# Optimization experiments

Measured on AMD Instinct MI355X. Metric: run time of the kernel, lower is better.

## Reference

```python
import jax, jax.numpy as jnp
from jax import lax
import numpy as np

B, C2, H2, W2 = 16, 512, 28, 28
C3, H3, W3 = 1024, 14, 14
N_CORESET, EMB = 16384, C2 + C3
IMG = 224
NUM_NEIGHBORS = 9
SIGMA = 4.0
KS = 2 * int(4.0 * SIGMA + 0.5) + 1  # kornia default kernel size = 33


def setup_inputs() -> dict:
    key = jax.random.key(0)
    k1, k2, k3 = jax.random.split(key, 3)
    return {
        "feat_layer2": jax.random.normal(k1, (B, C2, H2, W2), jnp.float32),
        "feat_layer3": jax.random.normal(k2, (B, C3, H3, W3), jnp.float32),
        "embedding_coreset": jax.random.normal(k3, (N_CORESET, EMB), jnp.float32),
    }


def avg_pool3(x):
    # torch.nn.AvgPool2d(3, 1, 1), count_include_pad=True -> always divide by 9
    s = lax.reduce_window(x, 0.0, lax.add, (1, 1, 3, 3), (1, 1, 1, 1),
                          [(0, 0), (0, 0), (1, 1), (1, 1)])
    return s / 9.0


def cdist(a, b):
    # euclidean cdist: [Q,E] x [N,E] -> [Q,N]
    a2 = jnp.sum(a * a, axis=-1, keepdims=True)          # [Q,1]
    b2 = jnp.sum(b * b, axis=-1)[None, :]                # [1,N]
    d2 = a2 + b2 - 2.0 * (a @ b.T)
    return jnp.sqrt(jnp.maximum(d2, 1e-12))


def gaussian_blur(x):
    # kornia GaussianBlur2d(kernel=33, sigma=4, border='reflect'), separable
    half = (KS - 1) // 2
    t = jnp.arange(KS, dtype=x.dtype) - half
    k = jnp.exp(-(t * t) / (2.0 * SIGMA * SIGMA))
    k = k / jnp.sum(k)
    xp = jnp.pad(x, ((0, 0), (0, 0), (half, half), (half, half)), mode="reflect")
    dn = ("NCHW", "OIHW", "NCHW")
    y = lax.conv_general_dilated(xp, k.reshape(1, 1, KS, 1), (1, 1), "VALID", dimension_numbers=dn)
    y = lax.conv_general_dilated(y, k.reshape(1, 1, 1, KS), (1, 1), "VALID", dimension_numbers=dn)
    return y


def reference(feat_layer2, feat_layer3, embedding_coreset):
    # 1. feature pooling (AvgPool2d(3,1,1)) on each backbone layer
    p2 = avg_pool3(feat_layer2)                           # [B,512,28,28]
    p3 = avg_pool3(feat_layer3)                           # [B,1024,14,14]
    p3u = jnp.repeat(jnp.repeat(p3, 2, axis=2), 2, axis=3)  # [B,1024,28,28]
    embedding = jnp.concatenate([p2, p3u], axis=1)        # [B,1536,28,28]
    b, e, w, h = embedding.shape
    x = embedding.transpose(0, 2, 3, 1).reshape(-1, e)    # [B*28*28, 1536]

    # 3. nearest neighbor (n_neighbors=1) against the coreset
    dists = cdist(x, embedding_coreset)                   # [Q, N]
    patch_scores = jnp.min(dists, axis=1).reshape(b, -1)  # [B, P]
    locations = jnp.argmin(dists, axis=1).reshape(b, -1)  # [B, P]

    # 4. image-level anomaly score with num_neighbors=9 reweighting
    bidx = jnp.arange(b)
    max_patches = jnp.argmax(patch_scores, axis=1)        # [B]
    mpf = x.reshape(b, w * h, e)[bidx, max_patches]       # [B, E]
    score = patch_scores[bidx, max_patches]               # [B]
    nn_index = locations[bidx, max_patches]               # [B]
    nn_sample = embedding_coreset[nn_index]               # [B, E]
    d2 = cdist(nn_sample, embedding_coreset)              # [B, N]
    _, support = lax.top_k(-d2, NUM_NEIGHBORS)            # smallest 9, ascending
    sup_feats = embedding_coreset[support]                # [B, 9, E]
    diff = mpf[:, None, :] - sup_feats
    d_sup = jnp.sqrt(jnp.maximum(jnp.sum(diff * diff, axis=-1), 1e-12))  # [B, 9]
    weights = (1.0 - jax.nn.softmax(d_sup, axis=1))[:, 0]
    anomaly_score = weights * score                       # [B]

    # 5. anomaly map: bilinear upsample + gaussian blur
    sm = patch_scores.reshape(b, 1, w, h)
    sm = jax.image.resize(sm, (b, 1, IMG, IMG), method="bilinear")
    anomaly_map = gaussian_blur(sm)                       # [B,1,224,224]
    return anomaly_map, anomaly_score
```

## Files before the change

### kernel.cpp

```cpp
#include <hip/hip_runtime.h>
#include <math.h>

typedef unsigned char u8;
typedef unsigned short u16;
typedef unsigned int u32;
typedef unsigned long long u64;
typedef __attribute__((ext_vector_type(8))) int int8v;
typedef __attribute__((ext_vector_type(4))) int int4v;
typedef __attribute__((ext_vector_type(4))) float f32x4;

#define B_IMG 16
#define EMB 1536
#define NPATCH 784
#define Q_TOT (B_IMG * NPATCH)
#define NCORE 16384
#define BK 128
#define IMG 224
#define KS 33
#define HALF 16
#define REFINE_W 12.0f

#define BM 256
#define BN 256
#define MBLK (Q_TOT / BM)
#define NBLK2 (NCORE / BN)
#define NHALF 256


__device__ __forceinline__ u32 fkey(float f) {
    u32 u = __float_as_uint(f);
    return (u & 0x80000000u) ? ~u : (u | 0x80000000u);
}
__device__ __forceinline__ float fkey_inv(u32 k) {
    u32 u = (k & 0x80000000u) ? (k ^ 0x80000000u) : ~k;
    return __uint_as_float(u);
}

__device__ __forceinline__ u32 f2e4m3(float f) {
    u32 x = __float_as_uint(f);
    u32 sign = (x >> 24) & 0x80u;
    x &= 0x7fffffffu;
    if (x >= 0x43E00000u) return sign | 0x7Eu;
    u32 e = x >> 23;
    if (e >= 121) {
        u32 m = x & 0x7fffffu;
        u32 keep = m >> 20;
        u32 rest = m & 0xFFFFFu;
        u32 rnd = (rest > 0x80000u) || (rest == 0x80000u && (keep & 1u));
        u32 mant = keep + rnd;
        u32 e4 = e - 120;
        if (mant == 8) { mant = 0; e4 += 1; }
        return sign | (e4 << 3) | mant;
    }
    float a = __uint_as_float(x);
    u32 q = (u32)(a * 512.0f + 0.5f);
    if (q > 7) return sign | 0x08u;
    return sign | q;
}

__device__ __forceinline__ void async_copy16(const void* gsrc, void* ldst) {
    auto g = reinterpret_cast<const __attribute__((address_space(1))) u32*>(
        reinterpret_cast<uintptr_t>(gsrc));
    auto l = reinterpret_cast<__attribute__((address_space(3))) u32*>(
        reinterpret_cast<uintptr_t>(ldst));
    __builtin_amdgcn_global_load_lds(g, l, 16, 0, 0);
}

__global__ void k_split_cs(const float* __restrict__ cs, u8* __restrict__ cs8,
                           float* __restrict__ b2) {
    __shared__ float sm[4];
    const int n = blockIdx.x;
    const int t = threadIdx.x;
    const size_t base = (size_t)n * EMB;
    float s = 0.f;
#pragma unroll
    for (int i = 0; i < 6; ++i) {
        const int e = t + i * 256;
        float v = cs[base + e];
        cs8[base + e] = (u8)f2e4m3(v);
        s += v * v;
    }
#pragma unroll
    for (int off = 32; off > 0; off >>= 1) s += __shfl_down(s, off, 64);
    if ((t & 63) == 0) sm[t >> 6] = s;
    __syncthreads();
    if (t == 0) b2[n] = sm[0] + sm[1] + sm[2] + sm[3];
}

__global__ void k_build_x(const float* __restrict__ f2, const float* __restrict__ f3,
                          u8* __restrict__ x8, float* __restrict__ xf) {
    __shared__ float tile[32][33];
    const int tx = threadIdx.x, ty = threadIdx.y;
    const int hw0 = blockIdx.x * 32;
    const int e0 = blockIdx.y * 32;
    const int b = blockIdx.z;
    const int hw = hw0 + tx;
    const bool ok = hw < NPATCH;
    const int h = hw / 28, w = hw - h * 28;
#pragma unroll
    for (int j = 0; j < 4; ++j) {
        const int el = ty + 8 * j;
        const int e = e0 + el;
        float v = 0.f;
        if (ok) {
            if (e < 512) {
                const float* p = f2 + (size_t)(b * 512 + e) * 784;
#pragma unroll
                for (int dy = -1; dy <= 1; ++dy) {
                    int yy = h + dy;
                    if (yy < 0 || yy >= 28) continue;
#pragma unroll
                    for (int dx = -1; dx <= 1; ++dx) {
                        int xx = w + dx;
                        if (xx < 0 || xx >= 28) continue;
                        v += p[yy * 28 + xx];
                    }
                }
            } else {
                const int c = e - 512;
                const int y3 = h >> 1, x3 = w >> 1;
                const float* p = f3 + (size_t)(b * 1024 + c) * 196;
#pragma unroll
                for (int dy = -1; dy <= 1; ++dy) {
                    int yy = y3 + dy;
                    if (yy < 0 || yy >= 14) continue;
#pragma unroll
                    for (int dx = -1; dx <= 1; ++dx) {
                        int xx = x3 + dx;
                        if (xx < 0 || xx >= 14) continue;
                        v += p[yy * 14 + xx];
                    }
                }
            }
            v *= (1.0f / 9.0f);
        }
        tile[el][tx] = v;
    }
    __syncthreads();
#pragma unroll
    for (int j = 0; j < 4; ++j) {
        const int hwl = ty + 8 * j;
        const int hw2 = hw0 + hwl;
        if (hw2 < NPATCH) {
            const int q = b * NPATCH + hw2;
            const float v = tile[tx][hwl];
            x8[(size_t)q * EMB + e0 + tx] = (u8)f2e4m3(v);
            xf[(size_t)q * EMB + e0 + tx] = v;
        }
    }
}

__global__ __launch_bounds__(512, 2) void k_gemm(
    const u8* __restrict__ x8, const u8* __restrict__ cs8,
    const float* __restrict__ b2, u64* __restrict__ cand) {
    __shared__ __align__(16) u8 sA0[BM * BK];
    __shared__ __align__(16) u8 sA1[BM * BK];
    __shared__ __align__(16) u8 sB0[BN * BK];
    __shared__ __align__(16) u8 sB1[BN * BK];

    const int tid = threadIdx.x;
    const int lane = tid & 63;
    const int wid = tid >> 6;
    const int wy = wid >> 2;
    const int wx = wid & 3;
    const int qd = lane >> 4;
    const int lr = lane & 15;
    const int sw = lr & 7;

    const u32 bid = blockIdx.x;
    const u32 xcd = bid & 7;
    const u32 sl = bid >> 3;
    const int bx = (int)(xcd * 8 + (sl & 7));
    const int by = (int)(sl >> 3);
    const int m0 = by * BM;
    const int n0 = bx * BN;

    size_t srcA[4], srcB[4];
    int dst[4];
#pragma unroll
    for (int j = 0; j < 4; ++j) {
        const int s = tid + j * 512;
        const int r = s >> 3, p = s & 7;
        const int col = (p ^ (r & 7)) << 4;
        srcA[j] = (size_t)(m0 + r) * EMB + col;
        srcB[j] = (size_t)(n0 + r) * EMB + col;
        dst[j] = s << 4;
    }

    f32x4 acc[8][4];
#pragma unroll
    for (int i = 0; i < 8; ++i)
#pragma unroll
        for (int j = 0; j < 4; ++j) acc[i][j] = (f32x4){0.f, 0.f, 0.f, 0.f};

    const int aoff0 = (wy * 128 + lr) * BK + (((qd * 2) ^ sw) << 4);
    const int boff0 = (wx * 64 + lr) * BK + (((qd * 2) ^ sw) << 4);

#define STAGE(SA, SB, KSI) do {                                                \
        const size_t kk_ = (size_t)(KSI) * BK;                                 \
        _Pragma("unroll")                                                      \
        for (int j_ = 0; j_ < 4; ++j_) {                                       \
            async_copy16(x8 + srcA[j_] + kk_, (SA) + dst[j_]);                 \
            async_copy16(cs8 + srcB[j_] + kk_, (SB) + dst[j_]);                \
        }                                                                      \
    } while (0)

#define COMPUTE(SA, SB) do {                                                   \
        int8v a_[8];                                                           \
        _Pragma("unroll")                                                      \
        for (int mi_ = 0; mi_ < 8; ++mi_) {                                    \
            const int o_ = aoff0 + mi_ * (16 * BK);                            \
            *(int4v*)&a_[mi_] = *(const int4v*)((SA) + o_);                    \
            *(((int4v*)&a_[mi_]) + 1) = *(const int4v*)((SA) + (o_ ^ 16));     \
        }                                                                      \
        _Pragma("unroll")                                                      \
        for (int nj_ = 0; nj_ < 4; ++nj_) {                                    \
            const int ob_ = boff0 + nj_ * (16 * BK);                           \
            int8v b_;                                                          \
            *(int4v*)&b_ = *(const int4v*)((SB) + ob_);                        \
            *(((int4v*)&b_) + 1) = *(const int4v*)((SB) + (ob_ ^ 16));         \
            _Pragma("unroll")                                                  \
            for (int mi_ = 0; mi_ < 8; ++mi_)                                  \
                acc[mi_][nj_] = __builtin_amdgcn_mfma_scale_f32_16x16x128_f8f6f4( \
                    a_[mi_], b_, acc[mi_][nj_], 0, 0, 0, 0x7F7F7F7F, 0, 0x7F7F7F7F); \
        }                                                                      \
    } while (0)

    STAGE(sA0, sB0, 0);
    __syncthreads();
    for (int ks = 0; ks < 12; ks += 2) {
        STAGE(sA1, sB1, ks + 1);
        COMPUTE(sA0, sB0);
        __syncthreads();
        if (ks + 2 < 12) STAGE(sA0, sB0, ks + 2);
        COMPUTE(sA1, sB1);
        __syncthreads();
    }
#undef STAGE
#undef COMPUTE

    float bb[4];
#pragma unroll
    for (int nj = 0; nj < 4; ++nj) bb[nj] = b2[n0 + wx * 64 + nj * 16 + lr];

#pragma unroll
    for (int mi = 0; mi < 8; ++mi) {
#pragma unroll
        for (int r = 0; r < 4; ++r) {
            u64 best = ~0ull;
#pragma unroll
            for (int nj = 0; nj < 4; ++nj) {
                const int n_g = n0 + wx * 64 + nj * 16 + lr;
                float v = bb[nj] - 2.0f * acc[mi][nj][r];
                u64 key = ((u64)fkey(v) << 32) | (u32)n_g;
                best = best < key ? best : key;
            }
#pragma unroll
            for (int s = 1; s < 16; s <<= 1) {
                u64 o = __shfl_xor(best, s, 64);
                best = best < o ? best : o;
            }
            if (lr == 0) {
                const int m_l = wy * 128 + mi * 16 + qd * 4 + r;
                cand[(size_t)(m0 + m_l) * NHALF + (bx * 4 + wx)] = best;
            }
        }
    }
}

__global__ void k_refine(const u64* __restrict__ cand, const float* __restrict__ xf,
                         const float* __restrict__ cs,
                         float* __restrict__ scores, int* __restrict__ locs) {
    __shared__ u64 keys[NHALF];
    __shared__ float sx[EMB];
    __shared__ float fred[256];
    __shared__ u64 ured[256];
    __shared__ int clist[16];
    __shared__ int ccount;
    __shared__ float s_a2, s_lim;
    const int row = blockIdx.x;
    const int t = threadIdx.x;
    keys[t] = cand[(size_t)row * NHALF + t];
    float p = 0.f;
    for (int e = t; e < EMB; e += 256) {
        float v = xf[(size_t)row * EMB + e];
        sx[e] = v;
        p += v * v;
    }
    fred[t] = p;
    if (t == 0) ccount = 0;
    __syncthreads();
    for (int s = 128; s > 0; s >>= 1) {
        if (t < s) fred[t] += fred[t + s];
        __syncthreads();
    }
    if (t == 0) s_a2 = fred[0];
    ured[t] = keys[t];
    __syncthreads();
    for (int s = 128; s > 0; s >>= 1) {
        if (t < s) { u64 o = ured[t + s]; if (o < ured[t]) ured[t] = o; }
        __syncthreads();
    }
    if (t == 0) s_lim = s_a2 + fkey_inv((u32)(ured[0] >> 32)) + REFINE_W;
    __syncthreads();
    {
        float d2a = s_a2 + fkey_inv((u32)(keys[t] >> 32));
        if (d2a <= s_lim) {
            int pos = atomicAdd(&ccount, 1);
            if (pos < 16) clist[pos] = (int)(keys[t] & 0xffffffffu);
        }
    }
    __syncthreads();
    const int nc = min(ccount, 16);
    u64 best = ~0ull;
    for (int i = 0; i < nc; ++i) {
        const int n = clist[i];
        const float* c = cs + (size_t)n * EMB;
        float q = 0.f;
        for (int e = t; e < EMB; e += 256) {
            float d = sx[e] - c[e];
            q += d * d;
        }
        fred[t] = q;
        __syncthreads();
        for (int s = 128; s > 0; s >>= 1) {
            if (t < s) fred[t] += fred[t + s];
            __syncthreads();
        }
        if (t == 0) {
            u64 key = ((u64)fkey(fred[0]) << 32) | (u32)n;
            best = best < key ? best : key;
        }
        __syncthreads();
    }
    if (t == 0) {
        float d2 = fkey_inv((u32)(best >> 32));
        scores[row] = sqrtf(fmaxf(d2, 1e-12f));
        locs[row] = (int)(best & 0xffffffffu);
    }
}

__global__ void k_argmax(const float* __restrict__ scores, const int* __restrict__ locs,
                         float* __restrict__ imgscore, int* __restrict__ nnidx,
                         int* __restrict__ qstar) {
    __shared__ u64 red[256];
    const int b = blockIdx.x, t = threadIdx.x;
    u64 best = 0;
    for (int p = t; p < NPATCH; p += 256) {
        u32 u = __float_as_uint(scores[b * NPATCH + p]);
        u64 key = ((u64)u << 32) | (u32)(0xFFFFFFFFu - (u32)p);
        best = best > key ? best : key;
    }
    red[t] = best;
    __syncthreads();
    for (int s = 128; s > 0; s >>= 1) {
        if (t < s) { u64 o = red[t + s]; if (o > red[t]) red[t] = o; }
        __syncthreads();
    }
    if (t == 0) {
        u64 k = red[0];
        int p = (int)(0xFFFFFFFFu - (u32)(k & 0xFFFFFFFFu));
        imgscore[b] = __uint_as_float((u32)(k >> 32));
        nnidx[b] = locs[b * NPATCH + p];
        qstar[b] = b * NPATCH + p;
    }
}

__global__ void k_d2nn(const float* __restrict__ cs, const int* __restrict__ nnidx,
                       float* __restrict__ dpart) {
    __shared__ float snn[16 * 384];
    const int t = threadIdx.x;
    const int nb = blockIdx.x & 63, ksl = blockIdx.x >> 6;
    const int n = nb * 256 + t;
    const int k0 = ksl * 384;
#pragma unroll
    for (int j = 0; j < 6; ++j) {
        int fid = t + j * 256;
        int row = fid / 96;
        int c4 = fid - row * 96;
        ((float4*)snn)[row * 96 + c4] =
            ((const float4*)(cs + (size_t)nnidx[row] * EMB + k0))[c4];
    }
    __syncthreads();
    float acc[16];
#pragma unroll
    for (int b = 0; b < 16; ++b) acc[b] = 0.f;
    const float4* csrow = (const float4*)(cs + (size_t)n * EMB + k0);
    for (int k4 = 0; k4 < 96; ++k4) {
        float4 c4 = csrow[k4];
#pragma unroll
        for (int b = 0; b < 16; ++b) {
            float4 nb4 = ((const float4*)snn)[b * 96 + k4];
            acc[b] += c4.x * nb4.x + c4.y * nb4.y + c4.z * nb4.z + c4.w * nb4.w;
        }
    }
#pragma unroll
    for (int b = 0; b < 16; ++b)
        dpart[((size_t)ksl * 16 + b) * NCORE + n] = acc[b];
}

__global__ void k_topk(const float* __restrict__ dpart, const float* __restrict__ b2,
                       const int* __restrict__ nnidx,
                       const float* __restrict__ cs, const float* __restrict__ xf,
                       const int* __restrict__ qstar, const float* __restrict__ imgscore,
                       float* __restrict__ out_scores) {
    __shared__ float sd2[NCORE];
    __shared__ int sel_idx[9];
    __shared__ float dsup[9];
    __shared__ u64 red[256];
    __shared__ float fred[256];
    const int b = blockIdx.x, t = threadIdx.x;
    const float bnn = b2[nnidx[b]];
    for (int n = t; n < NCORE; n += 256) {
        float dot = dpart[(0 * 16 + b) * NCORE + n] + dpart[(1 * 16 + b) * NCORE + n] +
                    dpart[(2 * 16 + b) * NCORE + n] + dpart[(3 * 16 + b) * NCORE + n];
        sd2[n] = bnn + b2[n] - 2.f * dot;
    }
    __syncthreads();

    for (int j = 0; j < 9; ++j) {
        u64 best = ~0ull;
        for (int n = t; n < NCORE; n += 256) {
            u64 key = ((u64)fkey(sd2[n]) << 32) | (u32)n;
            best = best < key ? best : key;
        }
        red[t] = best;
        __syncthreads();
        for (int s = 128; s > 0; s >>= 1) {
            if (t < s) { u64 o = red[t + s]; if (o < red[t]) red[t] = o; }
            __syncthreads();
        }
        if (t == 0) {
            int sel = (int)(red[0] & 0xffffffffu);
            sel_idx[j] = sel;
            sd2[sel] = __uint_as_float(0x7F800000u);
        }
        __syncthreads();
    }

    const int q = qstar[b];
    for (int j = 0; j < 9; ++j) {
        const int s = sel_idx[j];
        float p = 0.f;
        for (int e = t; e < EMB; e += 256) {
            float d = xf[(size_t)q * EMB + e] - cs[(size_t)s * EMB + e];
            p += d * d;
        }
        fred[t] = p;
        __syncthreads();
        for (int ss = 128; ss > 0; ss >>= 1) {
            if (t < ss) fred[t] += fred[t + ss];
            __syncthreads();
        }
        if (t == 0) dsup[j] = sqrtf(fmaxf(fred[0], 1e-12f));
        __syncthreads();
    }

    if (t == 0) {
        float m = dsup[0];
        for (int j = 1; j < 9; ++j) m = fmaxf(m, dsup[j]);
        float se = 0.f, e0 = 0.f;
        for (int j = 0; j < 9; ++j) {
            float e = expf(dsup[j] - m);
            se += e;
            if (j == 0) e0 = e;
        }
        out_scores[b] = (1.0f - e0 / se) * imgscore[b];
    }
}

__global__ void k_bilx(const float* __restrict__ scores, float* __restrict__ Sx) {
    int i = blockIdx.x * 256 + threadIdx.x;
    if (i >= B_IMG * 28 * IMG) return;
    int x = i % IMG;
    int br = i / IMG;
    int r = br % 28, b = br / 28;
    float cx = (x + 0.5f) * 0.125f - 0.5f;
    int x0 = (int)floorf(cx);
    float fx = cx - (float)x0;
    int x1 = min(max(x0 + 1, 0), 27);
    x0 = min(max(x0, 0), 27);
    const float* s = scores + b * NPATCH + r * 28;
    Sx[i] = (1.f - fx) * s[x0] + fx * s[x1];
}

__global__ void k_blur_vf(const float* __restrict__ Sx, float* __restrict__ out1) {
    __shared__ float wv[28];
    const int y = blockIdx.x, b = blockIdx.y, t = threadIdx.x;
    if (t < 28) wv[t] = 0.f;
    __syncthreads();
    if (t == 0) {
        float wsum = 0.f;
        for (int j = 0; j < KS; ++j) {
            float d = (float)(j - HALF);
            wsum += expf(-(d * d) / 32.0f);
        }
        for (int j = 0; j < KS; ++j) {
            int yy = y - HALF + j;
            yy = yy < 0 ? -yy : (yy > 223 ? 446 - yy : yy);
            float cy = (yy + 0.5f) * 0.125f - 0.5f;
            int y0 = (int)floorf(cy);
            float fy = cy - (float)y0;
            int y1 = min(max(y0 + 1, 0), 27);
            y0 = min(max(y0, 0), 27);
            float d = (float)(j - HALF);
            float wkj = expf(-(d * d) / 32.0f) / wsum;
            wv[y0] += (1.f - fy) * wkj;
            wv[y1] += fy * wkj;
        }
    }
    __syncthreads();
    if (t < IMG) {
        float acc = 0.f;
#pragma unroll
        for (int r = 0; r < 28; ++r) acc += wv[r] * Sx[(b * 28 + r) * IMG + t];
        out1[((size_t)b * IMG + y) * IMG + t] = acc;
    }
}

__global__ void k_blur_h(const float* __restrict__ out1, float* __restrict__ out) {
    __shared__ float row[IMG];
    __shared__ float wk[KS];
    const int y = blockIdx.x, b = blockIdx.y, t = threadIdx.x;
    if (t < IMG) row[t] = out1[((size_t)b * IMG + y) * IMG + t];
    if (t < KS) {
        float d = (float)(t - HALF);
        wk[t] = expf(-(d * d) / 32.0f);
    }
    __syncthreads();
    if (t < IMG) {
        float wsum = 0.f, acc = 0.f;
#pragma unroll
        for (int j = 0; j < KS; ++j) wsum += wk[j];
#pragma unroll
        for (int j = 0; j < KS; ++j) {
            int xx = t - HALF + j;
            xx = xx < 0 ? -xx : (xx > 223 ? 446 - xx : xx);
            acc += wk[j] * row[xx];
        }
        out[((size_t)b * IMG + y) * IMG + t] = acc / wsum;
    }
}

extern "C" void kernel_launch(void* const* d_in, const int* in_sizes, int n_in,
                              void* d_out, int out_size, void* d_ws, size_t ws_size,
                              hipStream_t stream) {
    const float* f2 = (const float*)d_in[0];
    const float* f3 = (const float*)d_in[1];
    const float* cs = (const float*)d_in[2];
    float* out = (float*)d_out;

    char* w = (char*)d_ws;
    auto alloc = [&](size_t bytes) {
        char* p = w;
        w += (bytes + 255) & ~(size_t)255;
        return p;
    };
    u8* x8 = (u8*)alloc((size_t)Q_TOT * EMB);
    float* xf = (float*)alloc((size_t)Q_TOT * EMB * 4);
    u8* cs8 = (u8*)alloc((size_t)NCORE * EMB);
    float* b2 = (float*)alloc(NCORE * 4);
    u64* cand = (u64*)alloc((size_t)Q_TOT * NHALF * 8);
    float* scores = (float*)alloc(Q_TOT * 4);
    int* locs = (int*)alloc(Q_TOT * 4);
    float* imgscore = (float*)alloc(B_IMG * 4);
    int* nnidx = (int*)alloc(B_IMG * 4);
    int* qstar = (int*)alloc(B_IMG * 4);
    float* dpart = (float*)alloc((size_t)4 * B_IMG * NCORE * 4);
    float* Sx = (float*)alloc((size_t)B_IMG * 28 * IMG * 4);
    float* map1 = (float*)alloc((size_t)B_IMG * IMG * IMG * 4);

    k_split_cs<<<NCORE, 256, 0, stream>>>(cs, cs8, b2);
    k_build_x<<<dim3(25, 48, 16), dim3(32, 8), 0, stream>>>(f2, f3, x8, xf);
    k_gemm<<<dim3(MBLK * NBLK2), 512, 0, stream>>>(x8, cs8, b2, cand);
    k_refine<<<Q_TOT, 256, 0, stream>>>(cand, xf, cs, scores, locs);
    k_argmax<<<16, 256, 0, stream>>>(scores, locs, imgscore, nnidx, qstar);
    k_d2nn<<<256, 256, 0, stream>>>(cs, nnidx, dpart);
    k_topk<<<16, 256, 0, stream>>>(dpart, b2, nnidx, cs, xf, qstar, imgscore,
                                   out + B_IMG * IMG * IMG);
    k_bilx<<<(B_IMG * 28 * IMG + 255) / 256, 256, 0, stream>>>(scores, Sx);
    k_blur_vf<<<dim3(IMG, B_IMG), 256, 0, stream>>>(Sx, map1);
    k_blur_h<<<dim3(IMG, B_IMG), 256, 0, stream>>>(map1, out);
}
```

Measured before the change: 1.043 ms.

## Interleave LDS loads and MFMA phases with barriers and priority bumps in GEMM loop

Restructures the double-buffered FP8 MFMA main loop so that each k-step issues its async copies, loads A fragments, then alternates B-fragment LDS loads and 8-MFMA groups separated by workgroup barriers and sched_barriers. It raises wave priority around MFMA bursts with s_setprio and waits on vmcnt explicitly before the final barrier. The aim is to keep waves in lockstep so LDS reads from some waves overlap MFMA work from others, ping-pong style. The cost is many extra s_barrier instructions per k-step, which could stall waves if occupancy is low.

```diff
diff --git a/kernel.cpp b/kernel.cpp
--- a/kernel.cpp
+++ b/kernel.cpp
@@ -196,48 +196,86 @@
     const int aoff0 = (wy * 128 + lr) * BK + (((qd * 2) ^ sw) << 4);
     const int boff0 = (wx * 64 + lr) * BK + (((qd * 2) ^ sw) << 4);
 
-#define STAGE(SA, SB, KSI) do {                                                \
-        const size_t kk_ = (size_t)(KSI) * BK;                                 \
+#define PHASE_BAR() do {                                                       \
+        __builtin_amdgcn_sched_barrier(0);                                     \
+        __builtin_amdgcn_s_barrier();                                          \
+        __builtin_amdgcn_sched_barrier(0);                                     \
+    } while (0)
+
+#define LOADB(BV, SB, NJ) do {                                                 \
+        const int ob_ = boff0 + (NJ) * (16 * BK);                              \
+        *(int4v*)&(BV) = *(const int4v*)((SB) + ob_);                          \
+        *(((int4v*)&(BV)) + 1) = *(const int4v*)((SB) + (ob_ ^ 16));           \
+    } while (0)
+
+#define MFMA8(AARR, BV, NJ) do {                                               \
+        __builtin_amdgcn_s_setprio(1);                                         \
         _Pragma("unroll")                                                      \
-        for (int j_ = 0; j_ < 4; ++j_) {                                       \
-            async_copy16(x8 + srcA[j_] + kk_, (SA) + dst[j_]);                 \
-            async_copy16(cs8 + srcB[j_] + kk_, (SB) + dst[j_]);                \
+        for (int mi_ = 0; mi_ < 8; ++mi_)                                      \
+            acc[mi_][NJ] = __builtin_amdgcn_mfma_scale_f32_16x16x128_f8f6f4(   \
+                (AARR)[mi_], BV, acc[mi_][NJ], 0, 0, 0, 0x7F7F7F7F, 0, 0x7F7F7F7F); \
+        __builtin_amdgcn_s_setprio(0);                                         \
+    } while (0)
+
+#define KSTEP(SRA, SRB, SWA, SWB, KN, DOSTAGE) do {                            \
+        if (DOSTAGE) {                                                         \
+            const size_t kk_ = (size_t)(KN) * BK;                              \
+            _Pragma("unroll")                                                  \
+            for (int j_ = 0; j_ < 4; ++j_) {                                   \
+                async_copy16(x8 + srcA[j_] + kk_, (SWA) + dst[j_]);            \
+                async_copy16(cs8 + srcB[j_] + kk_, (SWB) + dst[j_]);           \
+            }                                                                  \
         }                                                                      \
-    } while (0)
-
-#define COMPUTE(SA, SB) do {                                                   \
         int8v a_[8];                                                           \
         _Pragma("unroll")                                                      \
         for (int mi_ = 0; mi_ < 8; ++mi_) {                                    \
             const int o_ = aoff0 + mi_ * (16 * BK);                            \
-            *(int4v*)&a_[mi_] = *(const int4v*)((SA) + o_);                    \
-            *(((int4v*)&a_[mi_]) + 1) = *(const int4v*)((SA) + (o_ ^ 16));     \
+            *(int4v*)&a_[mi_] = *(const int4v*)((SRA) + o_);                   \
+            *(((int4v*)&a_[mi_]) + 1) = *(const int4v*)((SRA) + (o_ ^ 16));    \
         }                                                                      \
-        _Pragma("unroll")                                                      \
-        for (int nj_ = 0; nj_ < 4; ++nj_) {                                    \
-            const int ob_ = boff0 + nj_ * (16 * BK);                           \
-            int8v b_;                                                          \
-            *(int4v*)&b_ = *(const int4v*)((SB) + ob_);                        \
-            *(((int4v*)&b_) + 1) = *(const int4v*)((SB) + (ob_ ^ 16));         \
-            _Pragma("unroll")                                                  \
-            for (int mi_ = 0; mi_ < 8; ++mi_)                                  \
-                acc[mi_][nj_] = __builtin_amdgcn_mfma_scale_f32_16x16x128_f8f6f4( \
-                    a_[mi_], b_, acc[mi_][nj_], 0, 0, 0, 0x7F7F7F7F, 0, 0x7F7F7F7F); \
-        }                                                                      \
+        int8v b0_;                                                             \
+        LOADB(b0_, SRB, 0);                                                    \
+        PHASE_BAR();                                                           \
+        MFMA8(a_, b0_, 0);                                                     \
+        PHASE_BAR();                                                           \
+        int8v b1_;                                                             \
+        LOADB(b1_, SRB, 1);                                                    \
+        PHASE_BAR();                                                           \
+        MFMA8(a_, b1_, 1);                                                     \
+        PHASE_BAR();                                                           \
+        int8v b2_;                                                             \
+        LOADB(b2_, SRB, 2);                                                    \
+        PHASE_BAR();                                                           \
+        MFMA8(a_, b2_, 2);                                                     \
+        PHASE_BAR();                                                           \
+        int8v b3_;                                                             \
+        LOADB(b3_, SRB, 3);                                                    \
+        PHASE_BAR();                                                           \
+        MFMA8(a_, b3_, 3);                                                     \
+        __builtin_amdgcn_sched_barrier(0);                                     \
+        if (DOSTAGE) { asm volatile("s_waitcnt vmcnt(0)" ::: "memory"); }      \
+        __builtin_amdgcn_sched_barrier(0);                                     \
+        __builtin_amdgcn_s_barrier();                                          \
+        __builtin_amdgcn_sched_barrier(0);                                     \
     } while (0)
 
-    STAGE(sA0, sB0, 0);
-    __syncthreads();
+    {
+#pragma unroll
+        for (int j = 0; j < 4; ++j) {
+            async_copy16(x8 + srcA[j], sA0 + dst[j]);
+            async_copy16(cs8 + srcB[j], sB0 + dst[j]);
+        }
+        __syncthreads();
+    }
+
     for (int ks = 0; ks < 12; ks += 2) {
-        STAGE(sA1, sB1, ks + 1);
-        COMPUTE(sA0, sB0);
-        __syncthreads();
-        if (ks + 2 < 12) STAGE(sA0, sB0, ks + 2);
-        COMPUTE(sA1, sB1);
-        __syncthreads();
-    }
-#undef STAGE
-#undef COMPUTE
+        KSTEP(sA0, sB0, sA1, sB1, ks + 1, true);
+        KSTEP(sA1, sB1, sA0, sB0, ks + 2, (ks + 2 < 12));
+    }
+#undef KSTEP
+#undef MFMA8
+#undef LOADB
+#undef PHASE_BAR
 
     float bb[4];
 #pragma unroll
```

Measured after the change: 2.177 ms. +108.6%, slower.
